# Kernel optimization log

Measured on AMD Instinct MI355X. Metric: run time of the kernel, lower is better.

Reference implementation:

```python
import jax, jax.numpy as jnp
import numpy as np

B, S = 1, 2048
HIDDEN = 4096
NQ, NKV, HD = 32, 8, 128
EPS = 1e-06
THETA = 10000.0


def setup_inputs() -> dict:
    key = jax.random.key(0)
    k0, k1, k2 = jax.random.split(key, 3)
    hidden_states = jax.random.normal(k0, (B, S, HIDDEN), jnp.float32)
    Wqkv = jax.random.normal(k1, (HIDDEN, (NQ + 2 * NKV) * HD), jnp.float32) * 0.02
    Wo = jax.random.normal(k2, (NQ * HD, HIDDEN), jnp.float32) * 0.02
    q_gamma = jnp.ones((HD,), jnp.float32)
    k_gamma = jnp.ones((HD,), jnp.float32)
    positions = jnp.broadcast_to(jnp.arange(S, dtype=jnp.int32), (B, S))
    # neox-style rotary tables: half head_dim frequencies
    inv_freq = 1.0 / (THETA ** (jnp.arange(0, HD, 2, dtype=jnp.float32) / HD))  # [HD/2]
    ang = positions[..., None].astype(jnp.float32) * inv_freq                   # [B,S,HD/2]
    return {
        'positions': positions,
        'hidden_states': hidden_states,
        'Wqkv': Wqkv,
        'Wo': Wo,
        'q_gamma': q_gamma,
        'k_gamma': k_gamma,
        'cos': jnp.cos(ang),
        'sin': jnp.sin(ang),
    }


def _rmsnorm(x, gamma):
    # per-head RMSNorm over last dim (head_dim)
    return x * jax.lax.rsqrt(jnp.mean(x * x, axis=-1, keepdims=True) + EPS) * gamma


def _rope(x, cos, sin):
    # x: [B,S,h,HD], cos/sin: [B,S,HD/2]; rotate-half (neox) style
    x1, x2 = jnp.split(x, 2, axis=-1)
    c = cos[:, :, None, :]
    s = sin[:, :, None, :]
    return jnp.concatenate([x1 * c - x2 * s, x2 * c + x1 * s], axis=-1)


def reference(positions, hidden_states, Wqkv, Wo, q_gamma, k_gamma, cos, sin):
    b, s, _ = hidden_states.shape
    qkv = hidden_states @ Wqkv                                  # [B,S,(NQ+2NKV)*HD]
    q, k, v = jnp.split(qkv, [NQ * HD, (NQ + NKV) * HD], axis=-1)
    q = _rmsnorm(q.reshape(b, s, NQ, HD), q_gamma)
    k = _rmsnorm(k.reshape(b, s, NKV, HD), k_gamma)
    v = v.reshape(b, s, NKV, HD)
    q = _rope(q, cos, sin)
    k = _rope(k, cos, sin)
    R = NQ // NKV                                               # GQA group size
    qg = q.reshape(b, s, NKV, R, HD)
    scores = jnp.einsum('bsgrd,btgd->bgrst', qg, k) * (HD ** -0.5)
    causal = jnp.tril(jnp.ones((s, s), bool))
    scores = jnp.where(causal, scores, jnp.finfo(scores.dtype).min)
    probs = jax.nn.softmax(scores, axis=-1)
    attn = jnp.einsum('bgrst,btgd->bsgrd', probs, v).reshape(b, s, NQ * HD)
    return attn @ Wo
```

## Files before the change

kernel.cpp:

```cpp
#include <hip/hip_runtime.h>
#include <hip/hip_bf16.h>


#define S_LEN   2048
#define HIDDEN  4096
#define NQ      32
#define NKV     8
#define HD      128
#define QKV_DIM 6144
#define NQHD    4096
#define K_OFF   4096
#define V_OFF   5120
#define EPSF    1e-6f

typedef _Float16 half8 __attribute__((ext_vector_type(8)));
typedef _Float16 half4v __attribute__((ext_vector_type(4)));
typedef _Float16 half2v __attribute__((ext_vector_type(2)));
typedef float floatx4 __attribute__((ext_vector_type(4)));

__device__ __forceinline__ void gload_lds16(const void* g, void* l) {
    __builtin_amdgcn_global_load_lds(
        (const __attribute__((address_space(1))) unsigned int*)g,
        (__attribute__((address_space(3))) unsigned int*)l, 16, 0, 0);
}

__global__ __launch_bounds__(256) void conv_f32_f16(const float* __restrict__ src,
                                                    _Float16* __restrict__ dst) {
    const size_t i = ((size_t)blockIdx.x * 256 + threadIdx.x) * 8;
    float4 a = *(const float4*)(src + i);
    float4 b = *(const float4*)(src + i + 4);
    half8 h;
    h[0] = (_Float16)a.x; h[1] = (_Float16)a.y; h[2] = (_Float16)a.z; h[3] = (_Float16)a.w;
    h[4] = (_Float16)b.x; h[5] = (_Float16)b.y; h[6] = (_Float16)b.z; h[7] = (_Float16)b.w;
    *(half8*)(dst + i) = h;
}

__global__ __launch_bounds__(256) void conv_w_transpose(const float* __restrict__ src,
                                                        _Float16* __restrict__ dst,
                                                        int N, int K) {
    __shared__ float T[64][65];
    const int tid = threadIdx.x;
    const int n0 = blockIdx.x * 64, k0 = blockIdx.y * 64;
    const int rr = tid >> 4, cc = (tid & 15) * 4;
    #pragma unroll
    for (int l = 0; l < 4; ++l) {
        const int r = rr + l * 16;
        *(float4*)&T[r][cc] = *(const float4*)(src + (size_t)(k0 + r) * N + n0 + cc);
    }
    __syncthreads();
    #pragma unroll
    for (int l = 0; l < 4; ++l) {
        const int rn = rr + l * 16;
        half4v h;
        h[0] = (_Float16)T[cc + 0][rn];
        h[1] = (_Float16)T[cc + 1][rn];
        h[2] = (_Float16)T[cc + 2][rn];
        h[3] = (_Float16)T[cc + 3][rn];
        *(half4v*)(dst + (size_t)(n0 + rn) * K + k0 + cc) = h;
    }
}

template <typename CT>
__global__ __launch_bounds__(256, 2) void gemm_bt_db(const _Float16* __restrict__ A,
                                                     const _Float16* __restrict__ Bt,
                                                     CT* __restrict__ C,
                                                     int K, int ldc) {
    __shared__ _Float16 sA[2][128 * 64];
    __shared__ _Float16 sB[2][128 * 64];

    const int tid = threadIdx.x;
    const int wave = tid >> 6, lane = tid & 63;
    const int fl = lane & 15, quad = lane >> 4;
    const int m0 = blockIdx.y * 128, n0 = blockIdx.x * 128;
    const int wm = (wave >> 1) * 64, wn = (wave & 1) * 64;

    const int srow = lane >> 3;
    const int sch  = ((lane & 7) ^ srow) * 8;

    auto stage = [&](int p, int kt) {
        const int kb = kt * 64;
        #pragma unroll
        for (int i = 0; i < 4; ++i) {
            const int r0 = i * 32 + wave * 8;
            gload_lds16(A + (size_t)(m0 + r0 + srow) * K + kb + sch,
                        &sA[p][r0 * 64]);
            gload_lds16(Bt + (size_t)(n0 + r0 + srow) * K + kb + sch,
                        &sB[p][r0 * 64]);
        }
    };

    floatx4 acc[4][4] = {};

    stage(0, 0);
    stage(1, 1);

    const int cs0 = (quad ^ (fl & 7)) << 4;
    const int cs1 = ((4 + quad) ^ (fl & 7)) << 4;

    const int NT = K >> 6;
    for (int t = 0; t < NT; ++t) {
        if (t == NT - 1)
            asm volatile("s_waitcnt vmcnt(0)\n\ts_barrier" ::: "memory");
        else
            asm volatile("s_waitcnt vmcnt(8)\n\ts_barrier" ::: "memory");

        const char* Ab = (const char*)&sA[t & 1][0];
        const char* Bb = (const char*)&sB[t & 1][0];

        #pragma unroll
        for (int ks = 0; ks < 2; ++ks) {
            const int cs = ks ? cs1 : cs0;
            half8 af[4], bf[4];
            #pragma unroll
            for (int x = 0; x < 4; ++x) {
                af[x] = *(const half8*)(Ab + (wm + x * 16 + fl) * 128 + cs);
                bf[x] = *(const half8*)(Bb + (wn + x * 16 + fl) * 128 + cs);
            }
            __builtin_amdgcn_s_setprio(1);
            #pragma unroll
            for (int i = 0; i < 4; ++i)
                #pragma unroll
                for (int j = 0; j < 4; ++j)
                    acc[i][j] = __builtin_amdgcn_mfma_f32_16x16x32_f16(
                        af[i], bf[j], acc[i][j], 0, 0, 0);
            __builtin_amdgcn_s_setprio(0);
        }

        asm volatile("s_barrier" ::: "memory");
        if (t + 2 < NT) stage(t & 1, t + 2);
    }

    #pragma unroll
    for (int i = 0; i < 4; ++i)
        #pragma unroll
        for (int j = 0; j < 4; ++j)
            #pragma unroll
            for (int r = 0; r < 4; ++r)
                C[(size_t)(m0 + wm + i * 16 + quad * 4 + r) * ldc
                  + n0 + wn + j * 16 + fl] = (CT)acc[i][j][r];
}

__global__ __launch_bounds__(256) void rmsnorm_rope_w(_Float16* __restrict__ qkv,
                                                      const float* __restrict__ qg,
                                                      const float* __restrict__ kg,
                                                      const float* __restrict__ cosb,
                                                      const float* __restrict__ sinb) {
    const int s = blockIdx.x;
    const int wave = threadIdx.x >> 6, lane = threadIdx.x & 63;
    const float c  = cosb[s * 64 + lane];
    const float sn = sinb[s * 64 + lane];

    #pragma unroll
    for (int hi = 0; hi < 10; ++hi) {
        const int h = hi * 4 + wave;
        const bool isq = (h < NQ);
        _Float16* base = qkv + (size_t)s * QKV_DIM
                         + (isq ? h * HD : K_OFF + (h - NQ) * HD);
        float x1 = (float)base[lane];
        float x2 = (float)base[lane + 64];
        float ss = x1 * x1 + x2 * x2;
        #pragma unroll
        for (int o = 32; o; o >>= 1) ss += __shfl_xor(ss, o);
        float rms = rsqrtf(ss * (1.0f / (float)HD) + EPSF);
        const float* g = isq ? qg : kg;
        float xn1 = x1 * rms * g[lane];
        float xn2 = x2 * rms * g[lane + 64];
        base[lane]      = (_Float16)(xn1 * c - xn2 * sn);
        base[lane + 64] = (_Float16)(xn2 * c + xn1 * sn);
    }
}

#define FAM 32
#define FAN 64
#define LQK 136
#define LVP 68

__global__ __launch_bounds__(256, 2) void flash_attn_gqa(
        const _Float16* __restrict__ qkv, _Float16* __restrict__ attn) {
    __shared__ __align__(16) _Float16 Ks[FAN][LQK];
    __shared__ __align__(16) _Float16 Vt[HD][LVP];
    __shared__ __align__(16) _Float16 Ps[4][FAM][LVP];

    const int tid = threadIdx.x;
    const int wave = tid >> 6, lane = tid & 63;
    const int fl = lane & 15, quad = lane >> 4;

    const int bd = blockIdx.x;
    const int c = bd & 255, sflip = bd >> 8;
    const int qt = sflip ? 63 - (c & 63) : (c & 63);
    const int kvh = (sflip << 2) + (c >> 6);
    const int h = kvh * 4 + wave;
    const int m0 = qt * FAM;
    const float scale = 0.08838834764831845f;

    half8 qf[2][4];
    #pragma unroll
    for (int mt = 0; mt < 2; ++mt)
        #pragma unroll
        for (int ks = 0; ks < 4; ++ks)
            qf[mt][ks] = *(const half8*)(qkv
                + (size_t)(m0 + mt * 16 + fl) * QKV_DIM + h * HD + ks * 32 + quad * 8);

    float m_prev[2][4], l_prev[2][4];
    #pragma unroll
    for (int mt = 0; mt < 2; ++mt)
        #pragma unroll
        for (int r = 0; r < 4; ++r) { m_prev[mt][r] = -1e30f; l_prev[mt][r] = 0.f; }
    floatx4 oacc[2][8] = {};

    const int tmax = (m0 + FAM - 1) / FAN;
    for (int t = 0; t <= tmax; ++t) {
        const int n0 = t * FAN;
        __syncthreads();

        #pragma unroll
        for (int l = 0; l < 4; ++l) {
            const int f = tid + l * 256;
            const int r = f >> 4, c8 = (f & 15) * 8;
            *(half8*)&Ks[r][c8] = *(const half8*)(qkv
                + (size_t)(n0 + r) * QKV_DIM + K_OFF + kvh * HD + c8);
        }
        {
            const int p = tid & 31, g0 = tid >> 5;
            #pragma unroll
            for (int gi = 0; gi < 2; ++gi) {
                const int g = g0 + gi * 8;
                const _Float16* v0p = qkv + (size_t)(n0 + 2 * p) * QKV_DIM
                                      + V_OFF + kvh * HD + 8 * g;
                half8 va = *(const half8*)v0p;
                half8 vb = *(const half8*)(v0p + QKV_DIM);
                #pragma unroll
                for (int i = 0; i < 8; ++i) {
                    half2v hh; hh[0] = va[i]; hh[1] = vb[i];
                    *(half2v*)&Vt[8 * g + i][2 * p] = hh;
                }
            }
        }
        __syncthreads();

        floatx4 sacc[2][4] = {};
        __builtin_amdgcn_s_setprio(1);
        #pragma unroll
        for (int ks = 0; ks < 4; ++ks)
            #pragma unroll
            for (int nt = 0; nt < 4; ++nt) {
                half8 bf = *(const half8*)&Ks[nt * 16 + fl][ks * 32 + quad * 8];
                sacc[0][nt] = __builtin_amdgcn_mfma_f32_16x16x32_f16(
                    qf[0][ks], bf, sacc[0][nt], 0, 0, 0);
                sacc[1][nt] = __builtin_amdgcn_mfma_f32_16x16x32_f16(
                    qf[1][ks], bf, sacc[1][nt], 0, 0, 0);
            }
        __builtin_amdgcn_s_setprio(0);

        const bool diag = (t == tmax);
        float mx[2][4];
        #pragma unroll
        for (int mt = 0; mt < 2; ++mt)
            #pragma unroll
            for (int r = 0; r < 4; ++r) mx[mt][r] = -1e30f;
        #pragma unroll
        for (int mt = 0; mt < 2; ++mt)
            #pragma unroll
            for (int nt = 0; nt < 4; ++nt)
                #pragma unroll
                for (int r = 0; r < 4; ++r) {
                    float sv = sacc[mt][nt][r] * scale;
                    if (diag && (n0 + nt * 16 + fl > m0 + mt * 16 + quad * 4 + r))
                        sv = -1e30f;
                    sacc[mt][nt][r] = sv;
                    mx[mt][r] = fmaxf(mx[mt][r], sv);
                }
        #pragma unroll
        for (int mt = 0; mt < 2; ++mt)
            #pragma unroll
            for (int r = 0; r < 4; ++r)
                #pragma unroll
                for (int o = 8; o; o >>= 1)
                    mx[mt][r] = fmaxf(mx[mt][r], __shfl_xor(mx[mt][r], o));

        float alpha[2][4], rs[2][4];
        #pragma unroll
        for (int mt = 0; mt < 2; ++mt)
            #pragma unroll
            for (int r = 0; r < 4; ++r) {
                float nm = fmaxf(m_prev[mt][r], mx[mt][r]);
                alpha[mt][r] = __expf(m_prev[mt][r] - nm);
                m_prev[mt][r] = nm;
                rs[mt][r] = 0.f;
            }
        #pragma unroll
        for (int mt = 0; mt < 2; ++mt)
            #pragma unroll
            for (int nt = 0; nt < 4; ++nt)
                #pragma unroll
                for (int r = 0; r < 4; ++r) {
                    float p = __expf(sacc[mt][nt][r] - m_prev[mt][r]);
                    rs[mt][r] += p;
                    Ps[wave][mt * 16 + quad * 4 + r][nt * 16 + fl] = (_Float16)p;
                }
        #pragma unroll
        for (int mt = 0; mt < 2; ++mt)
            #pragma unroll
            for (int r = 0; r < 4; ++r) {
                #pragma unroll
                for (int o = 8; o; o >>= 1) rs[mt][r] += __shfl_xor(rs[mt][r], o);
                l_prev[mt][r] = l_prev[mt][r] * alpha[mt][r] + rs[mt][r];
            }
        #pragma unroll
        for (int mt = 0; mt < 2; ++mt)
            #pragma unroll
            for (int dt = 0; dt < 8; ++dt)
                #pragma unroll
                for (int r = 0; r < 4; ++r) oacc[mt][dt][r] *= alpha[mt][r];

        __builtin_amdgcn_s_setprio(1);
        #pragma unroll
        for (int ks2 = 0; ks2 < 2; ++ks2) {
            half8 pa[2];
            #pragma unroll
            for (int mt = 0; mt < 2; ++mt) {
                half4v plo = *(const half4v*)&Ps[wave][mt * 16 + fl][ks2 * 32 + quad * 8];
                half4v phi = *(const half4v*)&Ps[wave][mt * 16 + fl][ks2 * 32 + quad * 8 + 4];
                pa[mt] = __builtin_shufflevector(plo, phi, 0, 1, 2, 3, 4, 5, 6, 7);
            }
            #pragma unroll
            for (int dt = 0; dt < 8; ++dt) {
                half4v vlo = *(const half4v*)&Vt[dt * 16 + fl][ks2 * 32 + quad * 8];
                half4v vhi = *(const half4v*)&Vt[dt * 16 + fl][ks2 * 32 + quad * 8 + 4];
                half8 vb = __builtin_shufflevector(vlo, vhi, 0, 1, 2, 3, 4, 5, 6, 7);
                oacc[0][dt] = __builtin_amdgcn_mfma_f32_16x16x32_f16(
                    pa[0], vb, oacc[0][dt], 0, 0, 0);
                oacc[1][dt] = __builtin_amdgcn_mfma_f32_16x16x32_f16(
                    pa[1], vb, oacc[1][dt], 0, 0, 0);
            }
        }
        __builtin_amdgcn_s_setprio(0);
    }

    #pragma unroll
    for (int mt = 0; mt < 2; ++mt) {
        float linv[4];
        #pragma unroll
        for (int r = 0; r < 4; ++r) linv[r] = 1.0f / l_prev[mt][r];
        #pragma unroll
        for (int dt = 0; dt < 8; ++dt)
            #pragma unroll
            for (int r = 0; r < 4; ++r)
                attn[(size_t)(m0 + mt * 16 + quad * 4 + r) * NQHD
                     + h * HD + dt * 16 + fl] = (_Float16)(oacc[mt][dt][r] * linv[r]);
    }
}

extern "C" void kernel_launch(void* const* d_in, const int* in_sizes, int n_in,
                              void* d_out, int out_size, void* d_ws, size_t ws_size,
                              hipStream_t stream) {
    const float* hidden = (const float*)d_in[1];
    const float* Wqkv   = (const float*)d_in[2];
    const float* Wo     = (const float*)d_in[3];
    const float* qg     = (const float*)d_in[4];
    const float* kg     = (const float*)d_in[5];
    const float* cosb   = (const float*)d_in[6];
    const float* sinb   = (const float*)d_in[7];
    float* out = (float*)d_out;

    _Float16* buf0  = (_Float16*)d_ws;
    _Float16* wT    = buf0 + (size_t)S_LEN * HIDDEN;
    _Float16* qkv16 = (_Float16*)d_out;
    _Float16* attn16 = buf0;

    conv_f32_f16<<<(S_LEN * HIDDEN) / 2048, 256, 0, stream>>>(hidden, buf0);
    conv_w_transpose<<<dim3(QKV_DIM / 64, HIDDEN / 64), 256, 0, stream>>>(
        Wqkv, wT, QKV_DIM, HIDDEN);
    gemm_bt_db<_Float16><<<dim3(QKV_DIM / 128, S_LEN / 128), 256, 0, stream>>>(
        buf0, wT, qkv16, HIDDEN, QKV_DIM);
    rmsnorm_rope_w<<<S_LEN, 256, 0, stream>>>(qkv16, qg, kg, cosb, sinb);
    flash_attn_gqa<<<dim3((S_LEN / FAM) * NKV), 256, 0, stream>>>(qkv16, attn16);
    conv_w_transpose<<<dim3(HIDDEN / 64, NQHD / 64), 256, 0, stream>>>(
        Wo, wT, HIDDEN, NQHD);
    gemm_bt_db<float><<<dim3(HIDDEN / 128, S_LEN / 128), 256, 0, stream>>>(
        attn16, wT, out, NQHD, HIDDEN);
}
```

Before: 574.2 us.

## Replace GEMM with 512-thread 256-row tile kernel using phased load/MFMA interleave

Measured after the change: 547.5 us. -4.6%, faster.

```diff
diff --git a/kernel.cpp b/kernel.cpp
--- a/kernel.cpp
+++ b/kernel.cpp
@@ -60,85 +60,156 @@
     }
 }
 
-template <typename CT>
-__global__ __launch_bounds__(256, 2) void gemm_bt_db(const _Float16* __restrict__ A,
-                                                     const _Float16* __restrict__ Bt,
-                                                     CT* __restrict__ C,
-                                                     int K, int ldc) {
-    __shared__ _Float16 sA[2][128 * 64];
-    __shared__ _Float16 sB[2][128 * 64];
+#define MFMA_PH(MB, NB)                                                        \
+    asm volatile("s_waitcnt lgkmcnt(0)" ::: "memory");                         \
+    __builtin_amdgcn_sched_barrier(0);                                         \
+    __builtin_amdgcn_s_setprio(1);                                             \
+    _Pragma("unroll")                                                          \
+    for (int ks = 0; ks < 2; ++ks)                                             \
+        _Pragma("unroll")                                                      \
+        for (int mt = 0; mt < 4; ++mt)                                         \
+            _Pragma("unroll")                                                  \
+            for (int nt = 0; nt < 2; ++nt)                                     \
+                acc[(MB) + mt][(NB) + nt] =                                    \
+                    __builtin_amdgcn_mfma_f32_16x16x32_f16(                    \
+                        af[mt][ks], bf[(NB) + nt][ks],                         \
+                        acc[(MB) + mt][(NB) + nt], 0, 0, 0);                   \
+    __builtin_amdgcn_s_setprio(0);                                             \
+    __builtin_amdgcn_sched_barrier(0);
+
+#define READ_AF(H)                                                             \
+    _Pragma("unroll")                                                          \
+    for (int mt = 0; mt < 4; ++mt) {                                           \
+        const char* p_ = aB + ((H) * 64 + mt * 16 + fl) * 128;                 \
+        af[mt][0] = *(const half8*)(p_ + cs0);                                 \
+        af[mt][1] = *(const half8*)(p_ + cs1);                                 \
+    }
+
+#define READ_BF(NB)                                                            \
+    _Pragma("unroll")                                                          \
+    for (int j = 0; j < 2; ++j) {                                              \
+        const char* p_ = bB + (((NB) + j) * 16 + fl) * 128;                    \
+        bf[(NB) + j][0] = *(const half8*)(p_ + cs0);                           \
+        bf[(NB) + j][1] = *(const half8*)(p_ + cs1);                           \
+    }
+
+#define PHBAR asm volatile("s_barrier" ::: "memory")
+
+template <typename CT, int BN>
+__global__ __launch_bounds__(512, 2) void gemm_8ph(const _Float16* __restrict__ A,
+                                                   const _Float16* __restrict__ Bt,
+                                                   CT* __restrict__ C,
+                                                   int K, int ldc) {
+    constexpr int NI = BN / 64;
+    constexpr int NBH = BN / 128;
+
+    __shared__ _Float16 sA[2][2][128 * 64];
+    __shared__ _Float16 sB[2][NBH][128 * 64];
 
     const int tid = threadIdx.x;
     const int wave = tid >> 6, lane = tid & 63;
     const int fl = lane & 15, quad = lane >> 4;
-    const int m0 = blockIdx.y * 128, n0 = blockIdx.x * 128;
-    const int wm = (wave >> 1) * 64, wn = (wave & 1) * 64;
+    const int wmh = wave >> 2;
+    const int wn  = (wave & 3) * (BN / 4);
+
+    const int m0 = blockIdx.y * 256, n0 = blockIdx.x * BN;
 
     const int srow = lane >> 3;
     const int sch  = ((lane & 7) ^ srow) * 8;
 
-    auto stage = [&](int p, int kt) {
-        const int kb = kt * 64;
-        #pragma unroll
-        for (int i = 0; i < 4; ++i) {
-            const int r0 = i * 32 + wave * 8;
-            gload_lds16(A + (size_t)(m0 + r0 + srow) * K + kb + sch,
-                        &sA[p][r0 * 64]);
-            gload_lds16(Bt + (size_t)(n0 + r0 + srow) * K + kb + sch,
-                        &sB[p][r0 * 64]);
-        }
+    auto stA = [&](int buf, int kt, int h) {
+        const _Float16* s = A + (size_t)(m0 + h * 128 + wave * 8 + srow) * K
+                            + kt * 64 + sch;
+        _Float16* d = &sA[buf][h][(wave * 8) * 64];
+        gload_lds16(s, d);
+        gload_lds16(s + (size_t)64 * K, d + 64 * 64);
     };
-
-    floatx4 acc[4][4] = {};
-
-    stage(0, 0);
-    stage(1, 1);
-
+    auto stB = [&](int buf, int kt, int h) {
+        const _Float16* s = Bt + (size_t)(n0 + h * 128 + wave * 8 + srow) * K
+                            + kt * 64 + sch;
+        _Float16* d = &sB[buf][h][(wave * 8) * 64];
+        gload_lds16(s, d);
+        gload_lds16(s + (size_t)64 * K, d + 64 * 64);
+    };
+
+    floatx4 acc[8][NI] = {};
     const int cs0 = (quad ^ (fl & 7)) << 4;
     const int cs1 = ((4 + quad) ^ (fl & 7)) << 4;
 
+    if constexpr (BN == 256) {
+        stA(0, 0, 0); stA(0, 0, 1);
+        stB(0, 0, 0); stB(0, 0, 1);
+        stB(1, 1, 0); stB(1, 1, 1);
+    } else {
+        stA(0, 0, 0); stA(0, 0, 1);
+        stB(0, 0, 0);
+        stB(1, 1, 0);
+    }
+
     const int NT = K >> 6;
     for (int t = 0; t < NT; ++t) {
-        if (t == NT - 1)
-            asm volatile("s_waitcnt vmcnt(0)\n\ts_barrier" ::: "memory");
+        const int cur = t & 1;
+        const char* aB = (const char*)&sA[cur][wmh][0];
+        const char* bB = (BN == 256)
+            ? (const char*)&sB[cur][wn >> 7][0] + (size_t)(wn & 64) * 128
+            : (const char*)&sB[cur][0][0] + (size_t)wn * 128;
+
+        half8 af[4][2], bf[NI][2];
+
+        if constexpr (BN == 256)
+            asm volatile("s_waitcnt vmcnt(4)\n\ts_barrier" ::: "memory");
         else
-            asm volatile("s_waitcnt vmcnt(8)\n\ts_barrier" ::: "memory");
-
-        const char* Ab = (const char*)&sA[t & 1][0];
-        const char* Bb = (const char*)&sB[t & 1][0];
-
-        #pragma unroll
-        for (int ks = 0; ks < 2; ++ks) {
-            const int cs = ks ? cs1 : cs0;
-            half8 af[4], bf[4];
-            #pragma unroll
-            for (int x = 0; x < 4; ++x) {
-                af[x] = *(const half8*)(Ab + (wm + x * 16 + fl) * 128 + cs);
-                bf[x] = *(const half8*)(Bb + (wn + x * 16 + fl) * 128 + cs);
-            }
-            __builtin_amdgcn_s_setprio(1);
-            #pragma unroll
-            for (int i = 0; i < 4; ++i)
-                #pragma unroll
-                for (int j = 0; j < 4; ++j)
-                    acc[i][j] = __builtin_amdgcn_mfma_f32_16x16x32_f16(
-                        af[i], bf[j], acc[i][j], 0, 0, 0);
-            __builtin_amdgcn_s_setprio(0);
+            asm volatile("s_waitcnt vmcnt(2)\n\ts_barrier" ::: "memory");
+
+        if constexpr (BN == 256) {
+            READ_AF(0)
+            READ_BF(0)
+            if (t + 1 < NT) stA(cur ^ 1, t + 1, 0);
+            PHBAR;
+            MFMA_PH(0, 0)
+            PHBAR;
+            READ_BF(2)
+            if (t + 1 < NT) stA(cur ^ 1, t + 1, 1);
+            PHBAR;
+            MFMA_PH(0, 2)
+            PHBAR;
+            READ_AF(1)
+            if (t + 2 < NT) stB(cur, t + 2, 0);
+            PHBAR;
+            MFMA_PH(4, 0)
+            PHBAR;
+            if (t + 2 < NT) stB(cur, t + 2, 1);
+            PHBAR;
+            MFMA_PH(4, 2)
+        } else {
+            READ_AF(0)
+            READ_BF(0)
+            if (t + 1 < NT) stA(cur ^ 1, t + 1, 0);
+            PHBAR;
+            MFMA_PH(0, 0)
+            PHBAR;
+            READ_AF(1)
+            if (t + 1 < NT) stA(cur ^ 1, t + 1, 1);
+            if (t + 2 < NT) stB(cur, t + 2, 0);
+            PHBAR;
+            MFMA_PH(4, 0)
         }
-
-        asm volatile("s_barrier" ::: "memory");
-        if (t + 2 < NT) stage(t & 1, t + 2);
-    }
-
-    #pragma unroll
-    for (int i = 0; i < 4; ++i)
-        #pragma unroll
-        for (int j = 0; j < 4; ++j)
+    }
+
+    #pragma unroll
+    for (int mi = 0; mi < 8; ++mi)
+        #pragma unroll
+        for (int ni = 0; ni < NI; ++ni)
             #pragma unroll
             for (int r = 0; r < 4; ++r)
-                C[(size_t)(m0 + wm + i * 16 + quad * 4 + r) * ldc
-                  + n0 + wn + j * 16 + fl] = (CT)acc[i][j][r];
-}
+                C[(size_t)(m0 + wmh * 128 + mi * 16 + quad * 4 + r) * ldc
+                  + n0 + wn + ni * 16 + fl] = (CT)acc[mi][ni][r];
+}
+
+#undef MFMA_PH
+#undef READ_AF
+#undef READ_BF
+#undef PHBAR
 
 __global__ __launch_bounds__(256) void rmsnorm_rope_w(_Float16* __restrict__ qkv,
                                                       const float* __restrict__ qg,
@@ -371,12 +442,12 @@
     conv_f32_f16<<<(S_LEN * HIDDEN) / 2048, 256, 0, stream>>>(hidden, buf0);
     conv_w_transpose<<<dim3(QKV_DIM / 64, HIDDEN / 64), 256, 0, stream>>>(
         Wqkv, wT, QKV_DIM, HIDDEN);
-    gemm_bt_db<_Float16><<<dim3(QKV_DIM / 128, S_LEN / 128), 256, 0, stream>>>(
+    gemm_8ph<_Float16, 256><<<dim3(QKV_DIM / 256, S_LEN / 256), 512, 0, stream>>>(
         buf0, wT, qkv16, HIDDEN, QKV_DIM);
     rmsnorm_rope_w<<<S_LEN, 256, 0, stream>>>(qkv16, qg, kg, cosb, sinb);
     flash_attn_gqa<<<dim3((S_LEN / FAM) * NKV), 256, 0, stream>>>(qkv16, attn16);
     conv_w_transpose<<<dim3(HIDDEN / 64, NQHD / 64), 256, 0, stream>>>(
         Wo, wT, HIDDEN, NQHD);
-    gemm_bt_db<float><<<dim3(HIDDEN / 128, S_LEN / 128), 256, 0, stream>>>(
+    gemm_8ph<float, 128><<<dim3(HIDDEN / 128, S_LEN / 256), 512, 0, stream>>>(
         attn16, wT, out, NQHD, HIDDEN);
 }
```
